# Kernel tuning notes

Measured on AMD Instinct MI355X. Metric: run time of the kernel, lower is better.

The kernel has to match this reference:

```python
import jax, jax.numpy as jnp
import numpy as np

B, S, H, V, NL = 64, 2048, 512, 50257, 2

def setup_inputs() -> dict:
    key = jax.random.key(0)
    ks = jax.random.split(key, 20)
    s = 0.02
    return {
        "input_ids": jax.random.randint(ks[0], (B,), 0, V),
        "hidden": jax.random.normal(ks[1], (NL, B, H), jnp.float32),
        "block_attn_weights": jax.random.uniform(ks[2], (B, 32), jnp.float32),
        "encoder_outputs": jax.random.normal(ks[3], (B, S, H), jnp.float32),
        "n_blocks": 32,
        "emb": jax.random.normal(ks[4], (V, H), jnp.float32) * s,
        "attn_W": jax.random.normal(ks[5], (H, H), jnp.float32) * s,
        "attn_b": jnp.zeros((H,), jnp.float32),
        "W_ih0": jax.random.normal(ks[6], (3 * H, 2 * H), jnp.float32) * s,
        "W_hh0": jax.random.normal(ks[7], (3 * H, H), jnp.float32) * s,
        "b_ih0": jnp.zeros((3 * H,), jnp.float32),
        "b_hh0": jnp.zeros((3 * H,), jnp.float32),
        "W_ih1": jax.random.normal(ks[8], (3 * H, H), jnp.float32) * s,
        "W_hh1": jax.random.normal(ks[9], (3 * H, H), jnp.float32) * s,
        "b_ih1": jnp.zeros((3 * H,), jnp.float32),
        "b_hh1": jnp.zeros((3 * H,), jnp.float32),
        "out_W": jax.random.normal(ks[10], (V, 2 * H), jnp.float32) * s,
        "out_b": jnp.zeros((V,), jnp.float32),
    }

def _gru_cell(x, h, W_ih, W_hh, b_ih, b_hh):
    gx = x @ W_ih.T + b_ih            # [B, 3H]
    gh = h @ W_hh.T + b_hh            # [B, 3H]
    xr, xz, xn = jnp.split(gx, 3, axis=-1)
    hr, hz, hn = jnp.split(gh, 3, axis=-1)
    r = jax.nn.sigmoid(xr + hr)
    z = jax.nn.sigmoid(xz + hz)
    n = jnp.tanh(xn + r * hn)
    return (1.0 - z) * n + z * h

def reference(input_ids, hidden, block_attn_weights, encoder_outputs, n_blocks,
              emb, attn_W, attn_b, W_ih0, W_hh0, b_ih0, b_hh0,
              W_ih1, W_hh1, b_ih1, b_hh1, out_W, out_b):
    b, s, h = encoder_outputs.shape
    L = s // n_blocks
    eo = encoder_outputs.reshape(b, n_blocks, L, h)          # [B,N,L,H]
    # Luong general score: h_dec . (W e + b), per block
    energy = jnp.einsum('bnlh,gh->bnlg', eo, attn_W) + attn_b  # [B,N,L,H]
    scores = jnp.einsum('bh,bnlh->bnl', hidden[-1], energy)    # [B,N,L]
    attn_w = jax.nn.softmax(scores, axis=-1)                   # [B,N,L]
    block_ctx = jnp.einsum('bnl,bnlh->bnh', attn_w, eo)        # [B,N,H]
    context = jnp.einsum('bn,bnh->bh', block_attn_weights, block_ctx)  # [B,H]
    embedded = emb[input_ids]                                  # [B,H]
    x = jnp.concatenate([embedded, context], axis=-1)          # [B,2H]
    h0 = _gru_cell(x, hidden[0], W_ih0, W_hh0, b_ih0, b_hh0)
    h1 = _gru_cell(h0, hidden[1], W_ih1, W_hh1, b_ih1, b_hh1)
    new_hidden = jnp.stack([h0, h1], axis=0)                   # [NL,B,H]
    out_in = jnp.concatenate([h1, context], axis=-1)           # [B,2H]
    log_probs = jax.nn.log_softmax(out_in @ out_W.T + out_b, axis=-1)  # [B,V]
    return (log_probs, new_hidden, context, attn_w)
```

## Files before the change

### kernel.cpp

```cpp
#include <hip/hip_runtime.h>

#define B_  64
#define S_  2048
#define H_  512
#define V_  50257
#define NB_ 32
#define L_  64
#define H3_ 1536

typedef float  f32x4  __attribute__((ext_vector_type(4)));
typedef __bf16 bf16x8 __attribute__((ext_vector_type(8)));

struct alignas(16) U4 { unsigned int x, y, z, w; };

__device__ __forceinline__ unsigned int f2bf_bits(float f) {
  unsigned int u = __float_as_uint(f);
  return (u + 0x7fffu + ((u >> 16) & 1u)) >> 16;
}

__device__ __forceinline__ float wave_sum(float v) {
#pragma unroll
  for (int off = 32; off > 0; off >>= 1) v += __shfl_xor(v, off, 64);
  return v;
}

__global__ __launch_bounds__(128) void k_q(const float* __restrict__ hidden,
                                           const float* __restrict__ attn_W,
                                           float* __restrict__ q) {
  __shared__ float sh[4 * H_];
  int tid = threadIdx.x;
  int h  = blockIdx.x * 128 + tid;
  int b0 = blockIdx.y * 4;
  const float* h1 = hidden + B_ * H_;
  for (int i = tid; i < 4 * H_; i += 128) sh[i] = h1[b0 * H_ + i];
  __syncthreads();
  float acc[4] = {0.f, 0.f, 0.f, 0.f};
  for (int g = 0; g < H_; ++g) {
    float w = attn_W[(size_t)g * H_ + h];
#pragma unroll
    for (int bb = 0; bb < 4; ++bb) acc[bb] += sh[bb * H_ + g] * w;
  }
#pragma unroll
  for (int bb = 0; bb < 4; ++bb) q[(b0 + bb) * H_ + h] = acc[bb];
}

__global__ __launch_bounds__(256) void k_attn(
    const float* __restrict__ eo, const float* __restrict__ hidden,
    const float* __restrict__ attn_b, const float* __restrict__ q,
    float* __restrict__ bc, float* __restrict__ attnw_out) {
  __shared__ float sm[4], ss[4];
  __shared__ float shA[4][H_];
  int tid = threadIdx.x;
  int wv = tid >> 6, lane = tid & 63;
  int idx = blockIdx.x;
  int b = idx >> 5, n = idx & 31;

  const float4* qv = (const float4*)(q + (size_t)b * H_);
  float4 q0 = qv[lane], q1 = qv[64 + lane];

  const float4* hv = (const float4*)(hidden + (size_t)B_ * H_ + (size_t)b * H_);
  const float4* av = (const float4*)attn_b;
  float4 hx = hv[lane], hy = hv[64 + lane];
  float4 ax = av[lane], ay = av[64 + lane];
  float c0 = hx.x*ax.x + hx.y*ax.y + hx.z*ax.z + hx.w*ax.w
           + hy.x*ay.x + hy.y*ay.y + hy.z*ay.z + hy.w*ay.w;
  c0 = wave_sum(c0);

  const float4* ev = (const float4*)(eo + (size_t)(b * NB_ + n) * L_ * H_);
  float m = -1e30f, s = 0.f, myscore = 0.f;
  float4 A0 = {0,0,0,0}, A1 = {0,0,0,0};
  for (int lr = 0; lr < 16; ++lr) {
    int l = wv * 16 + lr;
    float4 e0 = ev[l * 128 + lane];
    float4 e1 = ev[l * 128 + 64 + lane];
    float p = e0.x*q0.x + e0.y*q0.y + e0.z*q0.z + e0.w*q0.w
            + e1.x*q1.x + e1.y*q1.y + e1.z*q1.z + e1.w*q1.w;
    p = wave_sum(p) + c0;
    if (lane == lr) myscore = p;
    float mnew  = fmaxf(m, p);
    float alpha = __expf(m - mnew);
    float w     = __expf(p - mnew);
    s = s * alpha + w;
    A0.x = A0.x*alpha + w*e0.x; A0.y = A0.y*alpha + w*e0.y;
    A0.z = A0.z*alpha + w*e0.z; A0.w = A0.w*alpha + w*e0.w;
    A1.x = A1.x*alpha + w*e1.x; A1.y = A1.y*alpha + w*e1.y;
    A1.z = A1.z*alpha + w*e1.z; A1.w = A1.w*alpha + w*e1.w;
    m = mnew;
  }
  if (lane == 0) { sm[wv] = m; ss[wv] = s; }
  __syncthreads();
  float m_g = fmaxf(fmaxf(sm[0], sm[1]), fmaxf(sm[2], sm[3]));
  float s_g = ss[0]*__expf(sm[0]-m_g) + ss[1]*__expf(sm[1]-m_g)
            + ss[2]*__expf(sm[2]-m_g) + ss[3]*__expf(sm[3]-m_g);
  float scale = __expf(m - m_g);
  float4* pa = (float4*)&shA[wv][0];
  float4 w0 = {A0.x*scale, A0.y*scale, A0.z*scale, A0.w*scale};
  float4 w1 = {A1.x*scale, A1.y*scale, A1.z*scale, A1.w*scale};
  pa[lane] = w0; pa[64 + lane] = w1;
  __syncthreads();
  float inv = 1.f / s_g;
  float2 sum = {0.f, 0.f};
#pragma unroll
  for (int w = 0; w < 4; ++w) {
    float2 v = ((float2*)&shA[w][0])[tid];
    sum.x += v.x; sum.y += v.y;
  }
  float2* bv = (float2*)(bc + (size_t)(b * NB_ + n) * H_);
  bv[tid] = (float2){sum.x * inv, sum.y * inv};
  if (lane < 16)
    attnw_out[(size_t)(b * NB_ + n) * L_ + wv * 16 + lane] =
        __expf(myscore - m_g) * inv;
}

__global__ __launch_bounds__(512) void k_prep(
    const int* __restrict__ ids, const float* __restrict__ hidden,
    const float* __restrict__ baw, const float* __restrict__ emb,
    const float* __restrict__ bc, float* __restrict__ ctx,
    unsigned short* __restrict__ xcatb, unsigned short* __restrict__ h0b,
    unsigned short* __restrict__ h1b, float* __restrict__ out_ctx) {
  int b = blockIdx.x, h = threadIdx.x;
  int id = ids[b];
  float ev = emb[(size_t)id * H_ + h];
  float acc = 0.f;
  for (int n = 0; n < NB_; ++n)
    acc += baw[b * NB_ + n] * bc[(size_t)(b * NB_ + n) * H_ + h];
  ctx[b * H_ + h]      = acc;
  out_ctx[b * H_ + h]  = acc;
  xcatb[b * 1024 + h]        = (unsigned short)f2bf_bits(ev);
  xcatb[b * 1024 + 512 + h]  = (unsigned short)f2bf_bits(acc);
  h0b[b * H_ + h] = (unsigned short)f2bf_bits(hidden[b * H_ + h]);
  h1b[b * H_ + h] = (unsigned short)f2bf_bits(hidden[B_ * H_ + b * H_ + h]);
}

__global__ __launch_bounds__(256) void k_mv2(
    const float* __restrict__ W1, const float* __restrict__ bias1,
    const unsigned short* __restrict__ A1, float* __restrict__ C1, int K1,
    const float* __restrict__ W2, const float* __restrict__ bias2,
    const unsigned short* __restrict__ A2, float* __restrict__ C2, int K2) {
  bool sec = blockIdx.x >= 96;
  const float* W = sec ? W2 : W1;
  const float* bias = sec ? bias2 : bias1;
  const unsigned short* A = sec ? A2 : A1;
  float* C = sec ? C2 : C1;
  int K = sec ? K2 : K1;
  int blk = sec ? blockIdx.x - 96 : blockIdx.x;

  int tid = threadIdx.x;
  int wv = tid >> 6, lane = tid & 63;
  int mrow = lane & 15, qd = lane >> 4;
  int j = blk * 16 + mrow;
  const unsigned short* ap = A + (size_t)(wv * 16 + mrow) * K + qd * 8;
  const float* wp = W + (size_t)j * K + qd * 8;
  f32x4 acc = (f32x4){0.f, 0.f, 0.f, 0.f};
  for (int k0 = 0; k0 < K; k0 += 32) {
    bf16x8 af = __builtin_bit_cast(bf16x8, *(const U4*)(ap + k0));
    float4 w0 = *(const float4*)(wp + k0);
    float4 w1 = *(const float4*)(wp + k0 + 4);
    U4 braw;
    braw.x = f2bf_bits(w0.x) | (f2bf_bits(w0.y) << 16);
    braw.y = f2bf_bits(w0.z) | (f2bf_bits(w0.w) << 16);
    braw.z = f2bf_bits(w1.x) | (f2bf_bits(w1.y) << 16);
    braw.w = f2bf_bits(w1.z) | (f2bf_bits(w1.w) << 16);
    bf16x8 bf = __builtin_bit_cast(bf16x8, braw);
    acc = __builtin_amdgcn_mfma_f32_16x16x32_bf16(af, bf, acc, 0, 0, 0);
  }
  float bv = bias[j];
#pragma unroll
  for (int r = 0; r < 4; ++r) {
    int brow = wv * 16 + qd * 4 + r;
    C[(size_t)brow * H3_ + j] = acc[r] + bv;
  }
}

__global__ __launch_bounds__(256) void k_out(
    const float* __restrict__ W, const float* __restrict__ bias,
    const unsigned short* __restrict__ A, float* __restrict__ C) {
  int tid = threadIdx.x;
  int wv = tid >> 6, lane = tid & 63;
  int mrow = lane & 15, qd = lane >> 4;
  int j = blockIdx.x * 64 + wv * 16 + mrow;
  int jc = j < V_ ? j : V_ - 1;
  const float* wp = W + (size_t)jc * 1024 + qd * 8;
  const unsigned short* ap = A + mrow * 1024 + qd * 8;
  f32x4 acc[4];
#pragma unroll
  for (int r = 0; r < 4; ++r) acc[r] = (f32x4){0.f, 0.f, 0.f, 0.f};
  for (int k0 = 0; k0 < 1024; k0 += 32) {
    float4 w0 = *(const float4*)(wp + k0);
    float4 w1 = *(const float4*)(wp + k0 + 4);
    U4 braw;
    braw.x = f2bf_bits(w0.x) | (f2bf_bits(w0.y) << 16);
    braw.y = f2bf_bits(w0.z) | (f2bf_bits(w0.w) << 16);
    braw.z = f2bf_bits(w1.x) | (f2bf_bits(w1.y) << 16);
    braw.w = f2bf_bits(w1.z) | (f2bf_bits(w1.w) << 16);
    bf16x8 bw = __builtin_bit_cast(bf16x8, braw);
#pragma unroll
    for (int r = 0; r < 4; ++r) {
      bf16x8 af = __builtin_bit_cast(bf16x8, *(const U4*)(ap + r * 16 * 1024 + k0));
      acc[r] = __builtin_amdgcn_mfma_f32_16x16x32_bf16(af, bw, acc[r], 0, 0, 0);
    }
  }
  if (j < V_) {
    float bv = bias[j];
#pragma unroll
    for (int r = 0; r < 4; ++r) {
#pragma unroll
      for (int g = 0; g < 4; ++g) {
        int brow = r * 16 + qd * 4 + g;
        C[(size_t)brow * V_ + j] = acc[r][g] + bv;
      }
    }
  }
}

__global__ __launch_bounds__(512) void k_gru(
    const float* __restrict__ gx, const float* __restrict__ gh,
    const float* __restrict__ hprev, float* __restrict__ hnew_out,
    unsigned short* __restrict__ hnew_bf, const float* __restrict__ ctx,
    unsigned short* __restrict__ outin) {
  int b = blockIdx.x, i = threadIdx.x;
  size_t g0 = (size_t)b * H3_ + i;
  float xr = gx[g0], xz = gx[g0 + 512], xn = gx[g0 + 1024];
  float hr = gh[g0], hz = gh[g0 + 512], hn = gh[g0 + 1024];
  float r  = 1.f / (1.f + __expf(-(xr + hr)));
  float z  = 1.f / (1.f + __expf(-(xz + hz)));
  float nn = tanhf(xn + r * hn);
  float hp = hprev[b * H_ + i];
  float h  = (1.f - z) * nn + z * hp;
  hnew_out[b * H_ + i] = h;
  hnew_bf[b * H_ + i]  = (unsigned short)f2bf_bits(h);
  if (outin) {
    outin[b * 1024 + i]       = (unsigned short)f2bf_bits(h);
    outin[b * 1024 + 512 + i] = (unsigned short)f2bf_bits(ctx[b * H_ + i]);
  }
}

__global__ __launch_bounds__(1024) void k_lsm(const float* __restrict__ logits,
                                              float* __restrict__ out) {
  int b = blockIdx.x, tid = threadIdx.x;
  int lane = tid & 63, wid = tid >> 6;
  const float* row = logits + (size_t)b * V_;
  __shared__ float red[16];
  float mx = -1e30f;
  for (int j = tid; j < V_; j += 1024) mx = fmaxf(mx, row[j]);
#pragma unroll
  for (int off = 32; off > 0; off >>= 1) mx = fmaxf(mx, __shfl_xor(mx, off, 64));
  if (lane == 0) red[wid] = mx;
  __syncthreads();
  if (tid == 0) {
    float v = red[0];
    for (int i = 1; i < 16; ++i) v = fmaxf(v, red[i]);
    red[0] = v;
  }
  __syncthreads();
  mx = red[0];
  __syncthreads();
  float s = 0.f;
  for (int j = tid; j < V_; j += 1024) s += __expf(row[j] - mx);
  s = wave_sum(s);
  if (lane == 0) red[wid] = s;
  __syncthreads();
  if (tid == 0) {
    float v = 0.f;
    for (int i = 0; i < 16; ++i) v += red[i];
    red[0] = logf(v);
  }
  __syncthreads();
  float lse = mx + red[0];
  for (int j = tid; j < V_; j += 1024) out[(size_t)b * V_ + j] = row[j] - lse;
}

extern "C" void kernel_launch(void* const* d_in, const int* in_sizes, int n_in,
                              void* d_out, int out_size, void* d_ws, size_t ws_size,
                              hipStream_t stream) {
  const int*   ids    = (const int*)d_in[0];
  const float* hidden = (const float*)d_in[1];
  const float* baw    = (const float*)d_in[2];
  const float* eo     = (const float*)d_in[3];
  const float* emb    = (const float*)d_in[5];
  const float* attn_W = (const float*)d_in[6];
  const float* attn_b = (const float*)d_in[7];
  const float* W_ih0  = (const float*)d_in[8];
  const float* W_hh0  = (const float*)d_in[9];
  const float* b_ih0  = (const float*)d_in[10];
  const float* b_hh0  = (const float*)d_in[11];
  const float* W_ih1  = (const float*)d_in[12];
  const float* W_hh1  = (const float*)d_in[13];
  const float* b_ih1  = (const float*)d_in[14];
  const float* b_hh1  = (const float*)d_in[15];
  const float* out_W  = (const float*)d_in[16];
  const float* out_b  = (const float*)d_in[17];
  float* out = (float*)d_out;

  char* ws = (char*)d_ws;
  float*          q      = (float*)(ws + 0);
  float*          bc     = (float*)(ws + 131072);
  float*          ctx    = (float*)(ws + 4325376);
  unsigned short* xcatb  = (unsigned short*)(ws + 4456448);
  unsigned short* h0b    = (unsigned short*)(ws + 4587520);
  unsigned short* h1b    = (unsigned short*)(ws + 4653056);
  unsigned short* h0nb   = (unsigned short*)(ws + 4718592);
  unsigned short* outinb = (unsigned short*)(ws + 4784128);
  float*          gx     = (float*)(ws + 4915200);
  float*          gh     = (float*)(ws + 5308416);
  float*          logits = (float*)(ws + 5701632);

  float* out_lp   = out;
  float* out_nh   = out + 3216448;
  float* out_ctx  = out + 3281984;
  float* out_attw = out + 3314752;

  k_q   <<<dim3(4, 16), 128, 0, stream>>>(hidden, attn_W, q);
  k_attn<<<2048, 256, 0, stream>>>(eo, hidden, attn_b, q, bc, out_attw);
  k_prep<<<64, 512, 0, stream>>>(ids, hidden, baw, emb, bc, ctx, xcatb, h0b, h1b, out_ctx);

  k_mv2<<<192, 256, 0, stream>>>(W_ih0, b_ih0, xcatb, gx, 1024,
                                 W_hh0, b_hh0, h0b,   gh, 512);
  k_gru<<<64, 512, 0, stream>>>(gx, gh, hidden, out_nh, h0nb,
                                (const float*)nullptr, (unsigned short*)nullptr);

  k_mv2<<<192, 256, 0, stream>>>(W_ih1, b_ih1, h0nb, gx, 512,
                                 W_hh1, b_hh1, h1b,  gh, 512);
  k_gru<<<64, 512, 0, stream>>>(gx, gh, hidden + B_ * H_, out_nh + B_ * H_, h0nb,
                                ctx, outinb);

  k_out<<<786, 256, 0, stream>>>(out_W, out_b, outinb, logits);
  k_lsm<<<64, 1024, 0, stream>>>(logits, out_lp);
}
```

Measured before the change: 701.3 us.

## Use nontemporal loads/stores, unroll attention loop, and single-pass online log-softmax

The attention kernel now processes two encoder rows per iteration with interleaved shuffle reductions, which adds memory-level parallelism, and reads the encoder stream with nontemporal loads. The output projection reads out_W with nontemporal loads so the streamed weights do not pollute cache. The log-softmax kernel merges its max and sum passes into one online pass with a merged reduction and writes its output with nontemporal stores, cutting one full read of the logits. The online update adds per-element branches and extra exps.

```diff
diff --git a/kernel.cpp b/kernel.cpp
--- a/kernel.cpp
+++ b/kernel.cpp
@@ -16,6 +16,10 @@
 __device__ __forceinline__ unsigned int f2bf_bits(float f) {
   unsigned int u = __float_as_uint(f);
   return (u + 0x7fffu + ((u >> 16) & 1u)) >> 16;
+}
+
+__device__ __forceinline__ f32x4 ntload4(const float* p) {
+  return __builtin_nontemporal_load((const f32x4*)p);
 }
 
 __device__ __forceinline__ float wave_sum(float v) {
@@ -55,36 +59,53 @@
   int idx = blockIdx.x;
   int b = idx >> 5, n = idx & 31;
 
-  const float4* qv = (const float4*)(q + (size_t)b * H_);
-  float4 q0 = qv[lane], q1 = qv[64 + lane];
-
-  const float4* hv = (const float4*)(hidden + (size_t)B_ * H_ + (size_t)b * H_);
-  const float4* av = (const float4*)attn_b;
-  float4 hx = hv[lane], hy = hv[64 + lane];
-  float4 ax = av[lane], ay = av[64 + lane];
+  f32x4 q0 = *(const f32x4*)(q + (size_t)b * H_ + lane * 4);
+  f32x4 q1 = *(const f32x4*)(q + (size_t)b * H_ + 256 + lane * 4);
+
+  const float* hp = hidden + (size_t)B_ * H_ + (size_t)b * H_;
+  f32x4 hx = *(const f32x4*)(hp + lane * 4);
+  f32x4 hy = *(const f32x4*)(hp + 256 + lane * 4);
+  f32x4 ax = *(const f32x4*)(attn_b + lane * 4);
+  f32x4 ay = *(const f32x4*)(attn_b + 256 + lane * 4);
   float c0 = hx.x*ax.x + hx.y*ax.y + hx.z*ax.z + hx.w*ax.w
            + hy.x*ay.x + hy.y*ay.y + hy.z*ay.z + hy.w*ay.w;
   c0 = wave_sum(c0);
 
-  const float4* ev = (const float4*)(eo + (size_t)(b * NB_ + n) * L_ * H_);
+  const float* eb = eo + (size_t)(b * NB_ + n) * L_ * H_;
   float m = -1e30f, s = 0.f, myscore = 0.f;
-  float4 A0 = {0,0,0,0}, A1 = {0,0,0,0};
-  for (int lr = 0; lr < 16; ++lr) {
-    int l = wv * 16 + lr;
-    float4 e0 = ev[l * 128 + lane];
-    float4 e1 = ev[l * 128 + 64 + lane];
-    float p = e0.x*q0.x + e0.y*q0.y + e0.z*q0.z + e0.w*q0.w
-            + e1.x*q1.x + e1.y*q1.y + e1.z*q1.z + e1.w*q1.w;
-    p = wave_sum(p) + c0;
-    if (lane == lr) myscore = p;
-    float mnew  = fmaxf(m, p);
+  f32x4 A0 = {0,0,0,0}, A1 = {0,0,0,0};
+  for (int lr = 0; lr < 16; lr += 2) {
+    const float* rA = eb + (size_t)(wv * 16 + lr) * H_;
+    const float* rB = rA + H_;
+    f32x4 a0 = ntload4(rA + lane * 4);
+    f32x4 a1 = ntload4(rA + 256 + lane * 4);
+    f32x4 b0 = ntload4(rB + lane * 4);
+    f32x4 b1 = ntload4(rB + 256 + lane * 4);
+    float pa = a0.x*q0.x + a0.y*q0.y + a0.z*q0.z + a0.w*q0.w
+             + a1.x*q1.x + a1.y*q1.y + a1.z*q1.z + a1.w*q1.w;
+    float pb = b0.x*q0.x + b0.y*q0.y + b0.z*q0.z + b0.w*q0.w
+             + b1.x*q1.x + b1.y*q1.y + b1.z*q1.z + b1.w*q1.w;
+#pragma unroll
+    for (int off = 32; off > 0; off >>= 1) {
+      pa += __shfl_xor(pa, off, 64);
+      pb += __shfl_xor(pb, off, 64);
+    }
+    pa += c0; pb += c0;
+    if (lane == lr)     myscore = pa;
+    if (lane == lr + 1) myscore = pb;
+    float mnew  = fmaxf(m, fmaxf(pa, pb));
     float alpha = __expf(m - mnew);
-    float w     = __expf(p - mnew);
-    s = s * alpha + w;
-    A0.x = A0.x*alpha + w*e0.x; A0.y = A0.y*alpha + w*e0.y;
-    A0.z = A0.z*alpha + w*e0.z; A0.w = A0.w*alpha + w*e0.w;
-    A1.x = A1.x*alpha + w*e1.x; A1.y = A1.y*alpha + w*e1.y;
-    A1.z = A1.z*alpha + w*e1.z; A1.w = A1.w*alpha + w*e1.w;
+    float wa    = __expf(pa - mnew);
+    float wb    = __expf(pb - mnew);
+    s = s * alpha + wa + wb;
+    A0.x = A0.x*alpha + wa*a0.x + wb*b0.x;
+    A0.y = A0.y*alpha + wa*a0.y + wb*b0.y;
+    A0.z = A0.z*alpha + wa*a0.z + wb*b0.z;
+    A0.w = A0.w*alpha + wa*a0.w + wb*b0.w;
+    A1.x = A1.x*alpha + wa*a1.x + wb*b1.x;
+    A1.y = A1.y*alpha + wa*a1.y + wb*b1.y;
+    A1.z = A1.z*alpha + wa*a1.z + wb*b1.z;
+    A1.w = A1.w*alpha + wa*a1.w + wb*b1.w;
     m = mnew;
   }
   if (lane == 0) { sm[wv] = m; ss[wv] = s; }
@@ -93,10 +114,10 @@
   float s_g = ss[0]*__expf(sm[0]-m_g) + ss[1]*__expf(sm[1]-m_g)
             + ss[2]*__expf(sm[2]-m_g) + ss[3]*__expf(sm[3]-m_g);
   float scale = __expf(m - m_g);
-  float4* pa = (float4*)&shA[wv][0];
-  float4 w0 = {A0.x*scale, A0.y*scale, A0.z*scale, A0.w*scale};
-  float4 w1 = {A1.x*scale, A1.y*scale, A1.z*scale, A1.w*scale};
-  pa[lane] = w0; pa[64 + lane] = w1;
+  f32x4* pa4 = (f32x4*)&shA[wv][0];
+  f32x4 w0 = {A0.x*scale, A0.y*scale, A0.z*scale, A0.w*scale};
+  f32x4 w1 = {A1.x*scale, A1.y*scale, A1.z*scale, A1.w*scale};
+  pa4[lane] = w0; pa4[64 + lane] = w1;
   __syncthreads();
   float inv = 1.f / s_g;
   float2 sum = {0.f, 0.f};
@@ -154,8 +175,8 @@
   f32x4 acc = (f32x4){0.f, 0.f, 0.f, 0.f};
   for (int k0 = 0; k0 < K; k0 += 32) {
     bf16x8 af = __builtin_bit_cast(bf16x8, *(const U4*)(ap + k0));
-    float4 w0 = *(const float4*)(wp + k0);
-    float4 w1 = *(const float4*)(wp + k0 + 4);
+    f32x4 w0 = *(const f32x4*)(wp + k0);
+    f32x4 w1 = *(const f32x4*)(wp + k0 + 4);
     U4 braw;
     braw.x = f2bf_bits(w0.x) | (f2bf_bits(w0.y) << 16);
     braw.y = f2bf_bits(w0.z) | (f2bf_bits(w0.w) << 16);
@@ -186,8 +207,8 @@
 #pragma unroll
   for (int r = 0; r < 4; ++r) acc[r] = (f32x4){0.f, 0.f, 0.f, 0.f};
   for (int k0 = 0; k0 < 1024; k0 += 32) {
-    float4 w0 = *(const float4*)(wp + k0);
-    float4 w1 = *(const float4*)(wp + k0 + 4);
+    f32x4 w0 = ntload4(wp + k0);
+    f32x4 w1 = ntload4(wp + k0 + 4);
     U4 braw;
     braw.x = f2bf_bits(w0.x) | (f2bf_bits(w0.y) << 16);
     braw.y = f2bf_bits(w0.z) | (f2bf_bits(w0.w) << 16);
@@ -240,34 +261,41 @@
   int b = blockIdx.x, tid = threadIdx.x;
   int lane = tid & 63, wid = tid >> 6;
   const float* row = logits + (size_t)b * V_;
-  __shared__ float red[16];
-  float mx = -1e30f;
-  for (int j = tid; j < V_; j += 1024) mx = fmaxf(mx, row[j]);
-#pragma unroll
-  for (int off = 32; off > 0; off >>= 1) mx = fmaxf(mx, __shfl_xor(mx, off, 64));
-  if (lane == 0) red[wid] = mx;
+  __shared__ float redm[16], reds[16], bl[1];
+  float m_t = -1e30f, s_t = 0.f;
+  for (int j = tid; j < V_; j += 1024) {
+    float x = row[j];
+    if (x > m_t) {
+      s_t = s_t * __expf(m_t - x) + 1.f;
+      m_t = x;
+    } else {
+      s_t += __expf(x - m_t);
+    }
+  }
+#pragma unroll
+  for (int off = 32; off > 0; off >>= 1) {
+    float mo = __shfl_xor(m_t, off, 64);
+    float so = __shfl_xor(s_t, off, 64);
+    float mn = fmaxf(m_t, mo);
+    s_t = s_t * __expf(m_t - mn) + so * __expf(mo - mn);
+    m_t = mn;
+  }
+  if (lane == 0) { redm[wid] = m_t; reds[wid] = s_t; }
   __syncthreads();
   if (tid == 0) {
-    float v = red[0];
-    for (int i = 1; i < 16; ++i) v = fmaxf(v, red[i]);
-    red[0] = v;
-  }
-  __syncthreads();
-  mx = red[0];
-  __syncthreads();
-  float s = 0.f;
-  for (int j = tid; j < V_; j += 1024) s += __expf(row[j] - mx);
-  s = wave_sum(s);
-  if (lane == 0) red[wid] = s;
-  __syncthreads();
-  if (tid == 0) {
-    float v = 0.f;
-    for (int i = 0; i < 16; ++i) v += red[i];
-    red[0] = logf(v);
-  }
-  __syncthreads();
-  float lse = mx + red[0];
-  for (int j = tid; j < V_; j += 1024) out[(size_t)b * V_ + j] = row[j] - lse;
+    float m_g = redm[0], s_g = reds[0];
+    for (int i = 1; i < 16; ++i) {
+      float mn = fmaxf(m_g, redm[i]);
+      s_g = s_g * __expf(m_g - mn) + reds[i] * __expf(redm[i] - mn);
+      m_g = mn;
+    }
+    bl[0] = m_g + logf(s_g);
+  }
+  __syncthreads();
+  float lse = bl[0];
+  float* orow = out + (size_t)b * V_;
+  for (int j = tid; j < V_; j += 1024)
+    __builtin_nontemporal_store(row[j] - lse, orow + j);
 }
 
 extern "C" void kernel_launch(void* const* d_in, const int* in_sizes, int n_in,
```

Result: no change. 691.2 us (-1.4%).
